# Kernel optimization log

Hardware: AMD Instinct MI355X
Metric: run time of the kernel (lower is better)

The kernel has to match this reference:

```python
import jax, jax.numpy as jnp
import numpy as np

HEADS = 16
DIM_HEAD = 64
SEG = 512
NPM = 16
RMS_EPS = 1.1920928955078125e-07  # torch.finfo(float32).eps, nn.RMSNorm default


def _rotate_half(x):
    # lucidrains rotary: adjacent pairs (x0, x1) -> (-x1, x0)
    x1 = x[..., 0::2]
    x2 = x[..., 1::2]
    return jnp.stack((-x2, x1), axis=-1).reshape(x.shape)


def _apply_rope(q, k):
    S = q.shape[-2]
    inv_freq = 1.0 / (10000.0 ** (jnp.arange(0, DIM_HEAD, 2, dtype=jnp.float32) / DIM_HEAD))
    freqs = jnp.arange(S, dtype=jnp.float32)[:, None] * inv_freq  # [S, Dh/2]
    freqs = jnp.repeat(freqs, 2, axis=-1)                          # [S, Dh] interleaved
    cos, sin = jnp.cos(freqs), jnp.sin(freqs)
    rot = lambda t: t * cos + _rotate_half(t) * sin
    return rot(q), rot(k)


def setup_inputs() -> dict:
    key = jax.random.key(0)
    ks = jax.random.split(key, 5)
    B, S, D = 2, 4096, 1024
    seq = jax.random.normal(ks[0], (B, S, D), dtype=jnp.float32)
    norm_weight = 1.0 + 0.02 * jax.random.normal(ks[1], (D,), dtype=jnp.float32)
    w_qkv = 0.02 * jax.random.normal(ks[2], (D, 3 * HEADS * DIM_HEAD), dtype=jnp.float32)
    w_out = 0.02 * jax.random.normal(ks[3], (HEADS * DIM_HEAD, D), dtype=jnp.float32)
    pmem = 0.02 * jax.random.normal(ks[4], (2, HEADS, NPM, DIM_HEAD), dtype=jnp.float32)
    return {"seq": seq, "norm_weight": norm_weight, "w_qkv": w_qkv, "w_out": w_out, "pmem": pmem}


def reference(seq, norm_weight, w_qkv, w_out, pmem):
    B, S, D = seq.shape
    W = S // SEG  # seq_len chosen as multiple of segment_len -> no padding

    # RMSNorm
    x = seq * jax.lax.rsqrt(jnp.mean(seq * seq, axis=-1, keepdims=True) + RMS_EPS) * norm_weight

    # QKV projection, split heads: [B, H, S, Dh]
    qkv = x @ w_qkv
    q, k, v = jnp.split(qkv, 3, axis=-1)
    split = lambda t: t.reshape(B, S, HEADS, DIM_HEAD).transpose(0, 2, 1, 3)
    q, k, v = split(q), split(k), split(v)
    orig_v = v

    # Rotary on full (unfolded) sequence positions
    q, k = _apply_rope(q, k)

    # Fold segments into batch: [B*W, H, SEG, Dh]
    fold = lambda t: t.reshape(B, HEADS, W, SEG, DIM_HEAD).transpose(0, 2, 1, 3, 4).reshape(B * W, HEADS, SEG, DIM_HEAD)
    q, k, v = fold(q), fold(k), fold(v)

    # Prepend persistent memory tokens to k/v
    pmk = jnp.broadcast_to(pmem[0], (B * W, HEADS, NPM, DIM_HEAD))
    pmv = jnp.broadcast_to(pmem[1], (B * W, HEADS, NPM, DIM_HEAD))
    k = jnp.concatenate((pmk, k), axis=-2)  # [B*W, H, NPM+SEG, Dh]
    v = jnp.concatenate((pmv, v), axis=-2)

    # Causal attention; persistent tokens (j < NPM) always visible
    scale = DIM_HEAD ** -0.5
    scores = jnp.einsum('bhid,bhjd->bhij', q, k) * scale  # [B*W, H, SEG, NPM+SEG]
    i_idx = jnp.arange(SEG)
    j_idx = jnp.arange(NPM + SEG)
    mask = (j_idx[None, :] - NPM) <= i_idx[:, None]
    scores = jnp.where(mask, scores, jnp.finfo(scores.dtype).min)
    attn = jax.nn.softmax(scores, axis=-1)
    out = jnp.einsum('bhij,bhjd->bhid', attn, v)  # [B*W, H, SEG, Dh]

    # Merge heads, output projection, unfold segments
    out = out.transpose(0, 2, 1, 3).reshape(B * W, SEG, HEADS * DIM_HEAD) @ w_out
    out = out.reshape(B, S, D)
    return out, orig_v
```

## Files before the change

### kernel.cpp

```cpp
#include <hip/hip_runtime.h>
#include <hip/hip_bf16.h>
#include <stdint.h>

#define HEADS 16
#define DIMH 64
#define SEGL 512
#define NPM 16
#define NB 2
#define NS 4096
#define ND 1024
#define NW 8
#define NBW 16
#define KVLEN 528
#define NQKV 3072
#define MROWS 8192
#define RMS_EPS 1.1920928955078125e-07f

typedef __attribute__((ext_vector_type(8))) short bf16x8;
typedef __attribute__((ext_vector_type(4))) float f32x4;
typedef __attribute__((ext_vector_type(8))) unsigned short u16x8;

union FragU { bf16x8 v; uint64_t q[2]; unsigned short u[8]; };

__device__ inline unsigned short f2bf(float x){
  __hip_bfloat16 b = __float2bfloat16(x);
  return __builtin_bit_cast(unsigned short, b);
}

__device__ inline f32x4 mfma16(bf16x8 a, bf16x8 b, f32x4 c){
  return __builtin_amdgcn_mfma_f32_16x16x32_bf16(a, b, c, 0, 0, 0);
}

__device__ __forceinline__ void gl_lds16(const unsigned short* g, unsigned short* l){
  __builtin_amdgcn_global_load_lds(
    (const __attribute__((address_space(1))) unsigned int*)g,
    (__attribute__((address_space(3))) unsigned int*)l, 16, 0, 0);
}

__device__ __forceinline__ void stage4(const unsigned short* gA, const unsigned short* gB,
                                       unsigned short* sA, unsigned short* sB, size_t row16){
  gl_lds16(gA,         sA);
  gl_lds16(gA + row16, sA + 512);
  gl_lds16(gB,         sB);
  gl_lds16(gB + row16, sB + 512);
}

__global__ void rope_table_k(float* __restrict__ cosT, float* __restrict__ sinT){
  int id = blockIdx.x*256 + threadIdx.x;
  if (id >= NS*32) return;
  int p = id & 31, s = id >> 5;
  float inv = powf(10000.0f, -(float)p * (1.0f/32.0f));
  float a = (float)s * inv;
  cosT[id] = cosf(a);
  sinT[id] = sinf(a);
}

__global__ __launch_bounds__(256) void rmsnorm_k(const float* __restrict__ seq, const float* __restrict__ nw,
                                                 unsigned short* __restrict__ xo){
  int r = blockIdx.x, t = threadIdx.x;
  const float4 v = ((const float4*)(seq + (size_t)r*ND))[t];
  float ss = v.x*v.x + v.y*v.y + v.z*v.z + v.w*v.w;
  #pragma unroll
  for (int off=32; off; off>>=1) ss += __shfl_xor(ss, off);
  __shared__ float red[4];
  if ((t&63)==0) red[t>>6] = ss;
  __syncthreads();
  float scale = rsqrtf((red[0]+red[1]+red[2]+red[3])*(1.0f/(float)ND) + RMS_EPS);
  const float4 w = ((const float4*)nw)[t];
  ushort4 o;
  o.x = f2bf(v.x*scale*w.x);
  o.y = f2bf(v.y*scale*w.y);
  o.z = f2bf(v.z*scale*w.z);
  o.w = f2bf(v.w*scale*w.w);
  ((ushort4*)xo)[(size_t)r*256 + t] = o;
}

__global__ __launch_bounds__(256) void tcast_k(const float* __restrict__ in, unsigned short* __restrict__ out,
                                               int R, int C){
  __shared__ float tile[32][33];
  int c0 = blockIdx.x*32, r0 = blockIdx.y*32;
  int tx = threadIdx.x & 31, ty = threadIdx.x >> 5;
  #pragma unroll
  for (int i=0;i<4;i++) tile[ty+8*i][tx] = in[(size_t)(r0+ty+8*i)*C + c0+tx];
  __syncthreads();
  #pragma unroll
  for (int i=0;i<4;i++) out[(size_t)(c0+ty+8*i)*R + r0+tx] = f2bf(tile[tx][ty+8*i]);
}

__global__ void pmem_fill_k(const float* __restrict__ pmem, unsigned short* __restrict__ Kb,
                            unsigned short* __restrict__ VbT){
  int id = blockIdx.x*256 + threadIdx.x;
  if (id >= NBW*HEADS*NPM*DIMH) return;
  int d = id & 63, j = (id>>6)&15, h = (id>>10)&15, bw = id>>14;
  size_t srcK = ((size_t)h*NPM + j)*DIMH + d;
  Kb[((size_t)(bw*HEADS+h)*KVLEN + j)*DIMH + d] = f2bf(pmem[srcK]);
  VbT[((size_t)(bw*HEADS+h)*DIMH + d)*KVLEN + j] = f2bf(pmem[(size_t)HEADS*NPM*DIMH + srcK]);
}

__global__ __launch_bounds__(256) void vtrans_k(const unsigned short* __restrict__ Vb,
                                                unsigned short* __restrict__ VbT){
  __shared__ unsigned short T[64][72];
  int jt = blockIdx.x, bwh = blockIdx.y, t = threadIdx.x;
  int r = t>>2, c = t&3;
  int j0 = jt*64;
  const unsigned short* src = Vb + ((size_t)bwh*512 + j0 + r)*DIMH + c*16;
  *(u16x8*)&T[r][c*16]     = *(const u16x8*)(src);
  *(u16x8*)&T[r][c*16 + 8] = *(const u16x8*)(src + 8);
  __syncthreads();
  u16x8 outv, outv2;
  #pragma unroll
  for (int k=0;k<8;k++) outv[k] = T[c*16+k][r];
  #pragma unroll
  for (int k=0;k<8;k++) outv2[k] = T[c*16+8+k][r];
  *(u16x8*)&VbT[((size_t)bwh*DIMH + r)*KVLEN + NPM + j0 + c*16] = outv;
  *(u16x8*)&VbT[((size_t)bwh*DIMH + r)*KVLEN + NPM + j0 + c*16 + 8] = outv2;
}

template<int MODE>
__device__ __forceinline__ void gemm_body(const unsigned short* __restrict__ A,
    const unsigned short* __restrict__ Bt, float* __restrict__ Cf,
    unsigned short* __restrict__ Qb, unsigned short* __restrict__ Kb, unsigned short* __restrict__ Vb,
    float* __restrict__ origv, const float* __restrict__ cosT, const float* __restrict__ sinT,
    int M, int N, int K){
  __shared__ __align__(16) unsigned short As[2][4096];
  __shared__ __align__(16) unsigned short Bs[2][4096];
  int t = threadIdx.x; int lane = t&63; int wv = t>>6; int lr = lane&15; int lg = lane>>4;
  int wm = wv>>1, wn = wv&1;
  int m0 = blockIdx.y*128, n0 = blockIdx.x*128;

  f32x4 acc[4][4];
  f32x4 z = {0.f,0.f,0.f,0.f};
  #pragma unroll
  for (int i=0;i<4;i++)
    #pragma unroll
    for (int j=0;j<4;j++) acc[i][j] = z;

  const unsigned short* gA = A  + (size_t)(m0 + wv*32 + (lane>>2))*K + (lane&3)*8;
  const unsigned short* gB = Bt + (size_t)(n0 + wv*32 + (lane>>2))*K + (lane&3)*8;
  const size_t row16 = (size_t)16*K;

  int aoff[4], boff[4];
  #pragma unroll
  for (int i=0;i<4;i++){
    aoff[i] = (wm*64 + i*16 + lr)*64 + lg*16;
    boff[i] = (wn*64 + i*16 + lr)*64 + lg*16;
  }

  stage4(gA, gB, As[0] + wv*1024, Bs[0] + wv*1024, row16);
  __syncthreads();

  int cur = 0;
  for (int k0=0; k0<K; k0+=32){
    int nk = k0 + 32;
    if (nk < K)
      stage4(gA + nk, gB + nk, As[cur^1] + wv*1024, Bs[cur^1] + wv*1024, row16);
    const char* AsB = (const char*)As[cur];
    const char* BsB = (const char*)Bs[cur];
    bf16x8 af[4], bfr[4];
    #pragma unroll
    for (int i=0;i<4;i++){
      af[i]  = *(const bf16x8*)(AsB + aoff[i]);
      bfr[i] = *(const bf16x8*)(BsB + boff[i]);
    }
    #pragma unroll
    for (int i=0;i<4;i++)
      #pragma unroll
      for (int j=0;j<4;j++)
        acc[i][j] = mfma16(af[i], bfr[j], acc[i][j]);
    __syncthreads();
    cur ^= 1;
  }

  #pragma unroll
  for (int i=0;i<4;i++){
    #pragma unroll
    for (int j=0;j<4;j++){
      if constexpr (MODE == 0){
        #pragma unroll
        for (int e=0;e<4;e++){
          int row = m0 + wm*64 + i*16 + lg*4 + e;
          int col = n0 + wn*64 + j*16 + lr;
          Cf[(size_t)row*N + col] = acc[i][j][e];
        }
      } else {
        int col  = n0 + wn*64 + j*16 + lr;
        int rowb = m0 + wm*64 + i*16 + lg*4;
        if (col < 2048){
          #pragma unroll
          for (int e=0;e<4;e++){
            int row = rowb + e;
            float val = acc[i][j][e];
            float partner = __shfl_xor(val, 1);
            int s = row&4095;
            int w = s>>9, ii = s&511, bwi = (row>>12)*8 + w;
            int hh = (col>>6)&15, dh = col&63;
            int fp = dh>>1;
            float cs = cosT[s*32+fp], sn = sinT[s*32+fp];
            float rot = (col&1) ? fmaf(val,cs, partner*sn) : fmaf(val,cs, -partner*sn);
            if (col < 1024) Qb[((size_t)(bwi*HEADS+hh)*SEGL + ii)*DIMH + dh] = f2bf(rot);
            else            Kb[((size_t)(bwi*HEADS+hh)*KVLEN + NPM + ii)*DIMH + dh] = f2bf(rot);
          }
        } else {
          #pragma unroll
          for (int e=0;e<4;e++){
            int row = rowb + e;
            float val = acc[i][j][e];
            int s = row&4095;
            int w = s>>9, ii = s&511, bwi = (row>>12)*8 + w;
            int hh = (col>>6)&15, dh = col&63;
            Vb[((size_t)(bwi*HEADS+hh)*512 + ii)*DIMH + dh] = f2bf(val);
            origv[((size_t)((row>>12)*HEADS+hh)*NS + s)*DIMH + dh] = val;
          }
        }
      }
    }
  }
}

__global__ __launch_bounds__(256) void gemm_qkv_k(const unsigned short* __restrict__ A,
    const unsigned short* __restrict__ Bt,
    unsigned short* __restrict__ Qb, unsigned short* __restrict__ Kb, unsigned short* __restrict__ Vb,
    float* __restrict__ origv, const float* __restrict__ cosT, const float* __restrict__ sinT){
  gemm_body<1>(A, Bt, nullptr, Qb, Kb, Vb, origv, cosT, sinT, MROWS, NQKV, 1024);
}

__global__ __launch_bounds__(256) void gemm_out_k(const unsigned short* __restrict__ A,
    const unsigned short* __restrict__ Bt, float* __restrict__ Cf){
  gemm_body<0>(A, Bt, Cf, nullptr, nullptr, nullptr, nullptr, nullptr, nullptr, MROWS, 1024, 1024);
}

__global__ __launch_bounds__(256) void attn_k(const unsigned short* __restrict__ Qb,
    const unsigned short* __restrict__ Kb, const unsigned short* __restrict__ VbT,
    unsigned short* __restrict__ att){
  int qt = blockIdx.x, h = blockIdx.y, bw = blockIdx.z;
  int t = threadIdx.x, lane = t&63, wv = t>>6, lr = lane&15, lg = lane>>4;
  __shared__ __align__(16) unsigned short Ks[2][4096];
  __shared__ __align__(16) unsigned short Vs[2][4096];

  const unsigned short* Kbase = Kb  + (size_t)(bw*HEADS+h)*KVLEN*DIMH;
  const unsigned short* Vtb   = VbT + (size_t)(bw*HEADS+h)*DIMH*KVLEN;

  bf16x8 qf[2][2];
  #pragma unroll
  for (int ifr=0; ifr<2; ++ifr){
    const unsigned short* Qrow = Qb + ((size_t)((bw*HEADS+h)*SEGL) + qt*128 + wv*32 + ifr*16 + lr)*DIMH;
    #pragma unroll
    for (int kh=0; kh<2; ++kh){
      FragU f;
      f.q[0] = *(const uint64_t*)(Qrow + kh*32 + lg*4);
      f.q[1] = *(const uint64_t*)(Qrow + kh*32 + 16 + lg*4);
      qf[ifr][kh] = f.v;
    }
  }

  int rls[2], xsw[2];
  #pragma unroll
  for (int k2=0;k2<2;k2++){
    rls[k2] = wv*16 + k2*8 + (lane>>3);
    xsw[k2] = ((lane&7)*16) ^ ((rls[k2]&7)<<4);
  }

  #define STAGE_KV(buf, j0_) do { \
    int xm_ = ((j0_) == 512) ? 31 : 127; \
    _Pragma("unroll") \
    for (int k2=0;k2<2;k2++){ \
      int jr = (j0_) + rls[k2]; if (jr>527) jr=527; \
      gl_lds16((const unsigned short*)((const char*)Kbase + (size_t)jr*128 + xsw[k2]), \
               Ks[buf] + wv*1024 + k2*512); \
      gl_lds16((const unsigned short*)((const char*)Vtb + (size_t)rls[k2]*(KVLEN*2) + (size_t)(j0_)*2 + (xsw[k2] & xm_)), \
               Vs[buf] + wv*1024 + k2*512); \
    } \
  } while(0)

  const float NEG = -3.0e38f;
  float m[2]  = {NEG, NEG};
  float lsum[2] = {0.f, 0.f};
  f32x4 o[4][2];
  f32x4 z = {0.f,0.f,0.f,0.f};
  #pragma unroll
  for (int df=0; df<4; ++df){ o[df][0]=z; o[df][1]=z; }

  int ntiles = (qt*128 + 207)>>6; if (ntiles>9) ntiles=9;
  int swzK = (lr&7)<<4;

  STAGE_KV(0, 0);
  __syncthreads();

  int cur = 0;
  for (int jt=0; jt<ntiles; ++jt){
    int j0 = jt*64;
    if (jt+1 < ntiles) STAGE_KV(cur^1, j0+64);

    const char* KsB = (const char*)Ks[cur];
    f32x4 s[2][4];
    #pragma unroll
    for (int ifr=0; ifr<2; ++ifr)
      #pragma unroll
      for (int jf=0; jf<4; ++jf) s[ifr][jf] = z;
    #pragma unroll
    for (int jf=0; jf<4; ++jf){
      int rowb = (jf*16 + lr)*128;
      #pragma unroll
      for (int kh=0; kh<2; ++kh){
        FragU kf;
        kf.q[0] = *(const uint64_t*)(KsB + rowb + ((kh*64      + lg*8) ^ swzK));
        kf.q[1] = *(const uint64_t*)(KsB + rowb + ((kh*64 + 32 + lg*8) ^ swzK));
        s[0][jf] = mfma16(kf.v, qf[0][kh], s[0][jf]);
        s[1][jf] = mfma16(kf.v, qf[1][kh], s[1][jf]);
      }
    }

    float alpha[2];
    #pragma unroll
    for (int ifr=0; ifr<2; ++ifr){
      int iglob = qt*128 + wv*32 + ifr*16 + lr;
      float mt = NEG;
      #pragma unroll
      for (int jf=0; jf<4; ++jf){
        #pragma unroll
        for (int e=0;e<4;e++){
          int jl = j0 + jf*16 + lg*4 + e;
          bool ok = (jl < KVLEN) && (jl - NPM <= iglob);
          float v = ok ? s[ifr][jf][e]*0.125f : NEG;
          s[ifr][jf][e] = v;
          mt = fmaxf(mt, v);
        }
      }
      mt = fmaxf(mt, __shfl_xor(mt, 16));
      mt = fmaxf(mt, __shfl_xor(mt, 32));
      float mn = fmaxf(m[ifr], mt);
      alpha[ifr] = __expf(m[ifr]-mn);
      m[ifr] = mn;
      float ps = 0.f;
      #pragma unroll
      for (int jf=0; jf<4; ++jf){
        #pragma unroll
        for (int e=0;e<4;e++){
          float p = __expf(s[ifr][jf][e] - mn);
          s[ifr][jf][e] = p;
          ps += p;
        }
      }
      ps += __shfl_xor(ps, 16);
      ps += __shfl_xor(ps, 32);
      lsum[ifr] = lsum[ifr]*alpha[ifr] + ps;
    }

    bf16x8 pa[2][2];
    #pragma unroll
    for (int ifr=0; ifr<2; ++ifr){
      #pragma unroll
      for (int kh=0; kh<2; ++kh){
        FragU f;
        #pragma unroll
        for (int e=0;e<4;e++){
          f.u[e]   = f2bf(s[ifr][2*kh  ][e]);
          f.u[4+e] = f2bf(s[ifr][2*kh+1][e]);
        }
        pa[ifr][kh] = f.v;
      }
    }

    #pragma unroll
    for (int ifr=0; ifr<2; ++ifr){
      float ae[4];
      #pragma unroll
      for (int e=0;e<4;e++) ae[e] = __shfl(alpha[ifr], lg*4+e, 16);
      #pragma unroll
      for (int df=0; df<4; ++df)
        #pragma unroll
        for (int e=0;e<4;e++) o[df][ifr][e] *= ae[e];
    }

    const char* VsB = (const char*)Vs[cur];
    #pragma unroll
    for (int df=0; df<4; ++df){
      int vrow = (df*16 + lr)*128;
      FragU v0, v1;
      v0.q[0] = *(const uint64_t*)(VsB + vrow + ((      lg*8) ^ swzK));
      v0.q[1] = *(const uint64_t*)(VsB + vrow + ((32  + lg*8) ^ swzK));
      v1.q[0] = *(const uint64_t*)(VsB + vrow + ((64  + lg*8) ^ swzK));
      v1.q[1] = *(const uint64_t*)(VsB + vrow + ((96  + lg*8) ^ swzK));
      o[df][0] = mfma16(pa[0][0], v0.v, o[df][0]);
      o[df][0] = mfma16(pa[0][1], v1.v, o[df][0]);
      o[df][1] = mfma16(pa[1][0], v0.v, o[df][1]);
      o[df][1] = mfma16(pa[1][1], v1.v, o[df][1]);
    }

    __syncthreads();
    cur ^= 1;
  }

  #pragma unroll
  for (int ifr=0; ifr<2; ++ifr){
    float inv = 1.0f / lsum[ifr];
    float il[4];
    #pragma unroll
    for (int e=0;e<4;e++) il[e] = __shfl(inv, lg*4+e, 16);
    #pragma unroll
    for (int e=0;e<4;e++){
      int row = bw*SEGL + qt*128 + wv*32 + ifr*16 + lg*4 + e;
      #pragma unroll
      for (int df=0; df<4; ++df)
        att[(size_t)row*1024 + h*64 + df*16 + lr] = f2bf(o[df][ifr][e]*il[e]);
    }
  }
  #undef STAGE_KV
}

extern "C" void kernel_launch(void* const* d_in, const int* in_sizes, int n_in,
                              void* d_out, int out_size, void* d_ws, size_t ws_size,
                              hipStream_t stream) {
  const float* seq  = (const float*)d_in[0];
  const float* nw   = (const float*)d_in[1];
  const float* wqkv = (const float*)d_in[2];
  const float* wout = (const float*)d_in[3];
  const float* pmem = (const float*)d_in[4];
  float* out0  = (float*)d_out;
  float* origv = out0 + (size_t)MROWS*ND;

  char* ws = (char*)d_ws;
  unsigned short* xbf   = (unsigned short*)(ws + 0);
  unsigned short* wqkvT = (unsigned short*)(ws + 16777216);
  unsigned short* woutT = (unsigned short*)(ws + 23068672);
  float*          cosT  = (float*)(ws + 25165824);
  float*          sinT  = (float*)(ws + 25690112);
  unsigned short* Qb    = (unsigned short*)(ws + 26214400);
  unsigned short* Kb    = (unsigned short*)(ws + 42991616);
  unsigned short* VbT   = (unsigned short*)(ws + 60293120);
  unsigned short* att   = (unsigned short*)(ws + 77594624);
  unsigned short* Vb    = att;

  rope_table_k<<<dim3(512), dim3(256), 0, stream>>>(cosT, sinT);
  rmsnorm_k<<<dim3(MROWS), dim3(256), 0, stream>>>(seq, nw, xbf);
  tcast_k<<<dim3(NQKV/32, 1024/32), dim3(256), 0, stream>>>(wqkv, wqkvT, 1024, NQKV);
  tcast_k<<<dim3(1024/32, 1024/32), dim3(256), 0, stream>>>(wout, woutT, 1024, 1024);
  pmem_fill_k<<<dim3(1024), dim3(256), 0, stream>>>(pmem, Kb, VbT);
  gemm_qkv_k<<<dim3(NQKV/128, MROWS/128), dim3(256), 0, stream>>>(
      xbf, wqkvT, Qb, Kb, Vb, origv, cosT, sinT);
  vtrans_k<<<dim3(8, NBW*HEADS), dim3(256), 0, stream>>>(Vb, VbT);
  attn_k<<<dim3(4, 16, 16), dim3(256), 0, stream>>>(Qb, Kb, VbT, att);
  gemm_out_k<<<dim3(1024/128, MROWS/128), dim3(256), 0, stream>>>(att, woutT, out0);
}
```

Before: 213.0 us.

## Rewrite QKV GEMM as 8-wave triple-buffered kernel with direct global-to-LDS loads

Replaces the QKV projection GEMM with a dedicated 512-thread kernel that computes 128x256 output tiles. It uses a three-stage LDS ring filled by direct global-to-LDS loads, XOR-swizzled LDS addressing, and a phased schedule that issues the next stages' loads while MFMAs run, with explicit waitcnt/barrier and setprio control. The aim is to hide global memory latency, avoid LDS bank conflicts and improve B-tile reuse. The cost is much more complex hand scheduling, and the larger block and LDS footprint may reduce occupancy. The output GEMM is split out unchanged.

```diff
diff --git a/kernel.cpp b/kernel.cpp
--- a/kernel.cpp
+++ b/kernel.cpp
@@ -116,12 +116,140 @@
   *(u16x8*)&VbT[((size_t)bwh*DIMH + r)*KVLEN + NPM + j0 + c*16 + 8] = outv2;
 }
 
-template<int MODE>
-__device__ __forceinline__ void gemm_body(const unsigned short* __restrict__ A,
-    const unsigned short* __restrict__ Bt, float* __restrict__ Cf,
+#define QNT 16
+
+__global__ __launch_bounds__(512) void gemm_qkv8_k(const unsigned short* __restrict__ A,
+    const unsigned short* __restrict__ Bt,
     unsigned short* __restrict__ Qb, unsigned short* __restrict__ Kb, unsigned short* __restrict__ Vb,
-    float* __restrict__ origv, const float* __restrict__ cosT, const float* __restrict__ sinT,
-    int M, int N, int K){
+    float* __restrict__ origv, const float* __restrict__ cosT, const float* __restrict__ sinT){
+  const int K = 1024;
+  __shared__ __align__(16) unsigned short As[3*128*64];
+  __shared__ __align__(16) unsigned short Bs[3*256*64];
+  int t0 = threadIdx.x; int lane = t0&63; int wv = t0>>6;
+  int lr = lane&15, lg = lane>>4;
+  int wm = wv>>2, wn = wv&3;
+  int m0 = blockIdx.y*128, n0 = blockIdx.x*256;
+  int swz = (lr&7)<<4;
+
+  f32x4 acc[4][4];
+  f32x4 z = {0.f,0.f,0.f,0.f};
+  #pragma unroll
+  for (int i=0;i<4;i++)
+    #pragma unroll
+    for (int j=0;j<4;j++) acc[i][j] = z;
+
+  int rbase = wv*8 + (lane>>3);
+  int kcs = ((lane&7)*8) ^ (((lane>>3)&7)*8);
+  const unsigned short* gA = A  + (size_t)(m0 + rbase)*K + kcs;
+  const unsigned short* gB = Bt + (size_t)(n0 + rbase)*K + kcs;
+  unsigned short* dA = As + wv*512;
+  unsigned short* dB = Bs + wv*512;
+
+#define SG_A(T_, BF_)  { gl_lds16(gA + (size_t)(T_)*64,               dA + (BF_)*8192); \
+                         gl_lds16(gA + (size_t)64*K  + (size_t)(T_)*64, dA + (BF_)*8192 + 4096); }
+#define SG_B01(T_, BF_){ gl_lds16(gB + (size_t)(T_)*64,               dB + (BF_)*16384); \
+                         gl_lds16(gB + (size_t)64*K  + (size_t)(T_)*64, dB + (BF_)*16384 + 4096); }
+#define SG_B23(T_, BF_){ gl_lds16(gB + (size_t)128*K + (size_t)(T_)*64, dB + (BF_)*16384 + 8192); \
+                         gl_lds16(gB + (size_t)192*K + (size_t)(T_)*64, dB + (BF_)*16384 + 12288); }
+
+  SG_A(0,0); SG_B01(0,0); SG_B23(0,0);
+  SG_A(1,1); SG_B01(1,1); SG_B23(1,1);
+  asm volatile("s_waitcnt vmcnt(6)" ::: "memory");
+  __builtin_amdgcn_s_barrier();
+  __builtin_amdgcn_sched_barrier(0);
+
+#define PH(MI, MJ, STAGE, TAILVM) do { \
+    FragU a_[2][2], b_[2][2]; \
+    _Pragma("unroll") \
+    for (int x=0;x<2;x++){ \
+      const char* pa = rA + (size_t)(wm*64 + (MI+x)*16 + lr)*128; \
+      const char* pb = rB + (size_t)(wn*64 + (MJ+x)*16 + lr)*128; \
+      _Pragma("unroll") \
+      for (int ks=0;ks<2;ks++){ \
+        a_[x][ks].q[0] = *(const uint64_t*)(pa + ((ks*64      + lg*8) ^ swz)); \
+        a_[x][ks].q[1] = *(const uint64_t*)(pa + ((ks*64 + 32 + lg*8) ^ swz)); \
+        b_[x][ks].q[0] = *(const uint64_t*)(pb + ((ks*64      + lg*8) ^ swz)); \
+        b_[x][ks].q[1] = *(const uint64_t*)(pb + ((ks*64 + 32 + lg*8) ^ swz)); \
+      } \
+    } \
+    STAGE; \
+    __builtin_amdgcn_s_barrier(); \
+    __builtin_amdgcn_sched_barrier(0); \
+    __builtin_amdgcn_s_setprio(1); \
+    _Pragma("unroll") \
+    for (int x=0;x<2;x++) \
+      _Pragma("unroll") \
+      for (int y=0;y<2;y++) \
+        _Pragma("unroll") \
+        for (int ks=0;ks<2;ks++) \
+          acc[MI+x][MJ+y] = mfma16(a_[x][ks].v, b_[y][ks].v, acc[MI+x][MJ+y]); \
+    __builtin_amdgcn_s_setprio(0); \
+    TAILVM; \
+    __builtin_amdgcn_s_barrier(); \
+    __builtin_amdgcn_sched_barrier(0); \
+  } while(0)
+
+  for (int t=0; t<QNT; ++t){
+    const char* rA = (const char*)(As + (t%3)*8192);
+    const char* rB = (const char*)(Bs + (t%3)*16384);
+    int b2 = (t+2)%3;
+    bool st = (t+2) < QNT;
+    PH(0,0, if(st){SG_A(t+2,b2);}, );
+    PH(0,2, if(st){SG_B01(t+2,b2);}, );
+    PH(2,0, if(st){SG_B23(t+2,b2);}, );
+    if (t < QNT-2){
+      PH(2,2, , { __builtin_amdgcn_sched_barrier(0); asm volatile("s_waitcnt vmcnt(6)" ::: "memory"); });
+    } else if (t == QNT-2){
+      PH(2,2, , { __builtin_amdgcn_sched_barrier(0); asm volatile("s_waitcnt vmcnt(0)" ::: "memory"); });
+    } else {
+      PH(2,2, , );
+    }
+  }
+#undef PH
+#undef SG_A
+#undef SG_B01
+#undef SG_B23
+
+  #pragma unroll
+  for (int i=0;i<4;i++){
+    #pragma unroll
+    for (int j=0;j<4;j++){
+      int col  = n0 + wn*64 + j*16 + lr;
+      int rowb = m0 + wm*64 + i*16 + lg*4;
+      if (col < 2048){
+        #pragma unroll
+        for (int e=0;e<4;e++){
+          int row = rowb + e;
+          float val = acc[i][j][e];
+          float partner = __shfl_xor(val, 1);
+          int s = row&4095;
+          int w = s>>9, ii = s&511, bwi = (row>>12)*8 + w;
+          int hh = (col>>6)&15, dh = col&63;
+          int fp = dh>>1;
+          float cs = cosT[s*32+fp], sn = sinT[s*32+fp];
+          float rot = (col&1) ? fmaf(val,cs, partner*sn) : fmaf(val,cs, -partner*sn);
+          if (col < 1024) Qb[((size_t)(bwi*HEADS+hh)*SEGL + ii)*DIMH + dh] = f2bf(rot);
+          else            Kb[((size_t)(bwi*HEADS+hh)*KVLEN + NPM + ii)*DIMH + dh] = f2bf(rot);
+        }
+      } else {
+        #pragma unroll
+        for (int e=0;e<4;e++){
+          int row = rowb + e;
+          float val = acc[i][j][e];
+          int s = row&4095;
+          int w = s>>9, ii = s&511, bwi = (row>>12)*8 + w;
+          int hh = (col>>6)&15, dh = col&63;
+          Vb[((size_t)(bwi*HEADS+hh)*512 + ii)*DIMH + dh] = f2bf(val);
+          origv[((size_t)((row>>12)*HEADS+hh)*NS + s)*DIMH + dh] = val;
+        }
+      }
+    }
+  }
+}
+
+__global__ __launch_bounds__(256) void gemm_out_k(const unsigned short* __restrict__ A,
+    const unsigned short* __restrict__ Bt, float* __restrict__ Cf){
+  const int M = MROWS, N = 1024, K = 1024;
   __shared__ __align__(16) unsigned short As[2][4096];
   __shared__ __align__(16) unsigned short Bs[2][4096];
   int t = threadIdx.x; int lane = t&63; int wv = t>>6; int lr = lane&15; int lg = lane>>4;
@@ -172,61 +300,15 @@
   }
 
   #pragma unroll
-  for (int i=0;i<4;i++){
-    #pragma unroll
-    for (int j=0;j<4;j++){
-      if constexpr (MODE == 0){
-        #pragma unroll
-        for (int e=0;e<4;e++){
-          int row = m0 + wm*64 + i*16 + lg*4 + e;
-          int col = n0 + wn*64 + j*16 + lr;
-          Cf[(size_t)row*N + col] = acc[i][j][e];
-        }
-      } else {
-        int col  = n0 + wn*64 + j*16 + lr;
-        int rowb = m0 + wm*64 + i*16 + lg*4;
-        if (col < 2048){
-          #pragma unroll
-          for (int e=0;e<4;e++){
-            int row = rowb + e;
-            float val = acc[i][j][e];
-            float partner = __shfl_xor(val, 1);
-            int s = row&4095;
-            int w = s>>9, ii = s&511, bwi = (row>>12)*8 + w;
-            int hh = (col>>6)&15, dh = col&63;
-            int fp = dh>>1;
-            float cs = cosT[s*32+fp], sn = sinT[s*32+fp];
-            float rot = (col&1) ? fmaf(val,cs, partner*sn) : fmaf(val,cs, -partner*sn);
-            if (col < 1024) Qb[((size_t)(bwi*HEADS+hh)*SEGL + ii)*DIMH + dh] = f2bf(rot);
-            else            Kb[((size_t)(bwi*HEADS+hh)*KVLEN + NPM + ii)*DIMH + dh] = f2bf(rot);
-          }
-        } else {
-          #pragma unroll
-          for (int e=0;e<4;e++){
-            int row = rowb + e;
-            float val = acc[i][j][e];
-            int s = row&4095;
-            int w = s>>9, ii = s&511, bwi = (row>>12)*8 + w;
-            int hh = (col>>6)&15, dh = col&63;
-            Vb[((size_t)(bwi*HEADS+hh)*512 + ii)*DIMH + dh] = f2bf(val);
-            origv[((size_t)((row>>12)*HEADS+hh)*NS + s)*DIMH + dh] = val;
-          }
-        }
+  for (int i=0;i<4;i++)
+    #pragma unroll
+    for (int j=0;j<4;j++)
+      #pragma unroll
+      for (int e=0;e<4;e++){
+        int row = m0 + wm*64 + i*16 + lg*4 + e;
+        int col = n0 + wn*64 + j*16 + lr;
+        Cf[(size_t)row*N + col] = acc[i][j][e];
       }
-    }
-  }
-}
-
-__global__ __launch_bounds__(256) void gemm_qkv_k(const unsigned short* __restrict__ A,
-    const unsigned short* __restrict__ Bt,
-    unsigned short* __restrict__ Qb, unsigned short* __restrict__ Kb, unsigned short* __restrict__ Vb,
-    float* __restrict__ origv, const float* __restrict__ cosT, const float* __restrict__ sinT){
-  gemm_body<1>(A, Bt, nullptr, Qb, Kb, Vb, origv, cosT, sinT, MROWS, NQKV, 1024);
-}
-
-__global__ __launch_bounds__(256) void gemm_out_k(const unsigned short* __restrict__ A,
-    const unsigned short* __restrict__ Bt, float* __restrict__ Cf){
-  gemm_body<0>(A, Bt, Cf, nullptr, nullptr, nullptr, nullptr, nullptr, nullptr, MROWS, 1024, 1024);
 }
 
 __global__ __launch_bounds__(256) void attn_k(const unsigned short* __restrict__ Qb,
@@ -436,7 +518,7 @@
   tcast_k<<<dim3(NQKV/32, 1024/32), dim3(256), 0, stream>>>(wqkv, wqkvT, 1024, NQKV);
   tcast_k<<<dim3(1024/32, 1024/32), dim3(256), 0, stream>>>(wout, woutT, 1024, 1024);
   pmem_fill_k<<<dim3(1024), dim3(256), 0, stream>>>(pmem, Kb, VbT);
-  gemm_qkv_k<<<dim3(NQKV/128, MROWS/128), dim3(256), 0, stream>>>(
+  gemm_qkv8_k<<<dim3(NQKV/256, MROWS/128), dim3(512), 0, stream>>>(
       xbf, wqkvT, Qb, Kb, Vb, origv, cosT, sinT);
   vtrans_k<<<dim3(8, NBW*HEADS), dim3(256), 0, stream>>>(Vb, VbT);
   attn_k<<<dim3(4, 16, 16), dim3(256), 0, stream>>>(Qb, Kb, VbT, att);
```

Measured after the change: 300.5 us. 1.41x slower.

## Deepen GEMM LDS pipeline to four stages with vmcnt-based waits

Applied to the files above, without the earlier changes.

The shared GEMM body now keeps four LDS buffers for A and B instead of two and prefetches three K-tiles ahead. The full __syncthreads is replaced by explicit s_waitcnt vmcnt counts plus s_barrier, so later loads can stay in flight while the current tile is computed. This is meant to hide global load latency in both the QKV and output projections. In exchange LDS use doubles to 64KB per block, which may reduce occupancy, and the hand-set vmcnt values depend on stage4 issuing exactly four loads.

```diff
diff --git a/kernel.cpp b/kernel.cpp
--- a/kernel.cpp
+++ b/kernel.cpp
@@ -121,10 +121,10 @@
     const unsigned short* __restrict__ Bt, float* __restrict__ Cf,
     unsigned short* __restrict__ Qb, unsigned short* __restrict__ Kb, unsigned short* __restrict__ Vb,
     float* __restrict__ origv, const float* __restrict__ cosT, const float* __restrict__ sinT,
-    int M, int N, int K){
-  __shared__ __align__(16) unsigned short As[2][4096];
-  __shared__ __align__(16) unsigned short Bs[2][4096];
-  int t = threadIdx.x; int lane = t&63; int wv = t>>6; int lr = lane&15; int lg = lane>>4;
+    int N, int K){
+  __shared__ __align__(16) unsigned short As[4][4096];
+  __shared__ __align__(16) unsigned short Bs[4][4096];
+  int t0 = threadIdx.x; int lane = t0&63; int wv = t0>>6; int lr = lane&15; int lg = lane>>4;
   int wm = wv>>1, wn = wv&1;
   int m0 = blockIdx.y*128, n0 = blockIdx.x*128;
 
@@ -146,16 +146,20 @@
     boff[i] = (wn*64 + i*16 + lr)*64 + lg*16;
   }
 
-  stage4(gA, gB, As[0] + wv*1024, Bs[0] + wv*1024, row16);
-  __syncthreads();
-
-  int cur = 0;
-  for (int k0=0; k0<K; k0+=32){
-    int nk = k0 + 32;
-    if (nk < K)
-      stage4(gA + nk, gB + nk, As[cur^1] + wv*1024, Bs[cur^1] + wv*1024, row16);
-    const char* AsB = (const char*)As[cur];
-    const char* BsB = (const char*)Bs[cur];
+  const int NT = K/32;
+  stage4(gA,      gB,      As[0] + wv*1024, Bs[0] + wv*1024, row16);
+  stage4(gA + 32, gB + 32, As[1] + wv*1024, Bs[1] + wv*1024, row16);
+  stage4(gA + 64, gB + 64, As[2] + wv*1024, Bs[2] + wv*1024, row16);
+  asm volatile("s_waitcnt vmcnt(8)" ::: "memory");
+  __builtin_amdgcn_s_barrier();
+  __builtin_amdgcn_sched_barrier(0);
+
+  for (int t=0; t<NT; ++t){
+    int k3 = (t+3)*32;
+    if (k3 < K)
+      stage4(gA + k3, gB + k3, As[(t+3)&3] + wv*1024, Bs[(t+3)&3] + wv*1024, row16);
+    const char* AsB = (const char*)As[t&3];
+    const char* BsB = (const char*)Bs[t&3];
     bf16x8 af[4], bfr[4];
     #pragma unroll
     for (int i=0;i<4;i++){
@@ -167,8 +171,13 @@
       #pragma unroll
       for (int j=0;j<4;j++)
         acc[i][j] = mfma16(af[i], bfr[j], acc[i][j]);
-    __syncthreads();
-    cur ^= 1;
+    if (t < NT-1){
+      if (t < NT-3)       asm volatile("s_waitcnt vmcnt(8)" ::: "memory");
+      else if (t == NT-3) asm volatile("s_waitcnt vmcnt(4)" ::: "memory");
+      else                asm volatile("s_waitcnt vmcnt(0)" ::: "memory");
+      __builtin_amdgcn_s_barrier();
+      __builtin_amdgcn_sched_barrier(0);
+    }
   }
 
   #pragma unroll
@@ -221,12 +230,12 @@
     const unsigned short* __restrict__ Bt,
     unsigned short* __restrict__ Qb, unsigned short* __restrict__ Kb, unsigned short* __restrict__ Vb,
     float* __restrict__ origv, const float* __restrict__ cosT, const float* __restrict__ sinT){
-  gemm_body<1>(A, Bt, nullptr, Qb, Kb, Vb, origv, cosT, sinT, MROWS, NQKV, 1024);
+  gemm_body<1>(A, Bt, nullptr, Qb, Kb, Vb, origv, cosT, sinT, NQKV, 1024);
 }
 
 __global__ __launch_bounds__(256) void gemm_out_k(const unsigned short* __restrict__ A,
     const unsigned short* __restrict__ Bt, float* __restrict__ Cf){
-  gemm_body<0>(A, Bt, Cf, nullptr, nullptr, nullptr, nullptr, nullptr, nullptr, MROWS, 1024, 1024);
+  gemm_body<0>(A, Bt, Cf, nullptr, nullptr, nullptr, nullptr, nullptr, nullptr, 1024, 1024);
 }
 
 __global__ __launch_bounds__(256) void attn_k(const unsigned short* __restrict__ Qb,
```

Result: slower. 242.2 us (+13.7%).
